# Kernel optimization log

Measured on AMD Instinct MI355X. Metric: run time of the kernel, lower is better.

The kernel has to match this reference:

```python
import math
import jax, jax.numpy as jnp
import numpy as np

B, H, W, C = 16, 64, 64, 192
WS, SHIFT, NH = 16, 8, 6
D = C // NH
N = WS * WS
HID = 4 * C
EPS = 1e-5


def _static_tables():
    # relative position index (N, N)
    coords = np.stack(np.meshgrid(np.arange(WS), np.arange(WS), indexing='ij'))  # (2, WS, WS)
    cf = coords.reshape(2, -1)
    rel = (cf[:, :, None] - cf[:, None, :]).transpose(1, 2, 0)  # (N, N, 2)
    rel[:, :, 0] += WS - 1
    rel[:, :, 1] += WS - 1
    rel[:, :, 0] *= 2 * WS - 1
    rel_idx = rel.sum(-1)  # (N, N)
    # log-spaced continuous relative coords table ((2WS-1)^2, 2)
    r = np.arange(-(WS - 1), WS, dtype=np.float32)
    tab = np.stack(np.meshgrid(r, r, indexing='ij'), axis=-1)  # (2WS-1, 2WS-1, 2)
    tab = tab / (WS - 1) * 8.0
    tab = np.sign(tab) * np.log2(np.abs(tab) + 1.0) / np.log2(8.0)
    # shifted-window attention mask (nW, N, N)
    img = np.zeros((H, W))
    cnt = 0
    for hs in (slice(0, -WS), slice(-WS, -SHIFT), slice(-SHIFT, None)):
        for ws_ in (slice(0, -WS), slice(-WS, -SHIFT), slice(-SHIFT, None)):
            img[hs, ws_] = cnt
            cnt += 1
    win = img.reshape(H // WS, WS, W // WS, WS).transpose(0, 2, 1, 3).reshape(-1, N)
    diff = win[:, None, :] - win[:, :, None]
    mask = np.where(diff != 0, -100.0, 0.0).astype(np.float32)
    return jnp.asarray(rel_idx), jnp.asarray(tab.reshape(-1, 2)), jnp.asarray(mask)

REL_IDX, CPB_TABLE, ATTN_MASK = _static_tables()


def setup_inputs() -> dict:
    key = jax.random.key(0)
    ks = jax.random.split(key, 24)
    s = 0.02
    return {
        'hidden_states': jax.random.normal(ks[0], (B, H * W, C), jnp.float32),
        'time': jax.random.uniform(ks[1], (B,), jnp.float32),
        'q_w': jax.random.normal(ks[2], (C, C), jnp.float32) * s,
        'q_b': jnp.zeros((C,), jnp.float32),
        'k_w': jax.random.normal(ks[3], (C, C), jnp.float32) * s,
        'v_w': jax.random.normal(ks[4], (C, C), jnp.float32) * s,
        'v_b': jnp.zeros((C,), jnp.float32),
        'logit_scale': jnp.full((NH, 1, 1), math.log(10.0), jnp.float32),
        'cpb_w1': jax.random.normal(ks[5], (512, 2), jnp.float32) * s,
        'cpb_b1': jnp.zeros((512,), jnp.float32),
        'cpb_w2': jax.random.normal(ks[6], (NH, 512), jnp.float32) * s,
        'proj_w': jax.random.normal(ks[7], (C, C), jnp.float32) * s,
        'proj_b': jnp.zeros((C,), jnp.float32),
        'ln1_ww': jax.random.normal(ks[8], (C, 1), jnp.float32) * s,
        'ln1_wb': jnp.ones((C,), jnp.float32),
        'ln1_bw': jax.random.normal(ks[9], (C, 1), jnp.float32) * s,
        'ln1_bb': jnp.zeros((C,), jnp.float32),
        'fc1_w': jax.random.normal(ks[10], (HID, C), jnp.float32) * s,
        'fc1_b': jnp.zeros((HID,), jnp.float32),
        'fc2_w': jax.random.normal(ks[11], (C, HID), jnp.float32) * s,
        'fc2_b': jnp.zeros((C,), jnp.float32),
        'ln2_ww': jax.random.normal(ks[12], (C, 1), jnp.float32) * s,
        'ln2_wb': jnp.ones((C,), jnp.float32),
        'ln2_bw': jax.random.normal(ks[13], (C, 1), jnp.float32) * s,
        'ln2_bb': jnp.zeros((C,), jnp.float32),
    }


def _cond_ln(x, time, ww, wb, bw, bb):
    mean = x.mean(-1, keepdims=True)
    var = (x ** 2).mean(-1, keepdims=True) - mean ** 2
    xn = (x - mean) / jnp.sqrt(var + EPS)
    t = time.reshape(-1, 1)
    w = (t @ ww.T + wb)[:, None, :]
    b = (t @ bw.T + bb)[:, None, :]
    return w * xn + b


def _forward(hidden_states, time, q_w, q_b, k_w, v_w, v_b, logit_scale,
             cpb_w1, cpb_b1, cpb_w2, proj_w, proj_b,
             ln1_ww, ln1_wb, ln1_bw, ln1_bb,
             fc1_w, fc1_b, fc2_w, fc2_b,
             ln2_ww, ln2_wb, ln2_bw, ln2_bb):
    nWh, nWw = H // WS, W // WS
    nW = nWh * nWw
    x = hidden_states.reshape(B, H, W, C)
    x = jnp.roll(x, (-SHIFT, -SHIFT), axis=(1, 2))
    # window partition -> (B*nW, N, C)
    xw = x.reshape(B, nWh, WS, nWw, WS, C).transpose(0, 1, 3, 2, 4, 5).reshape(-1, N, C)
    q = (xw @ q_w.T + q_b).reshape(-1, N, NH, D).transpose(0, 2, 1, 3)
    k = (xw @ k_w.T).reshape(-1, N, NH, D).transpose(0, 2, 1, 3)
    v = (xw @ v_w.T + v_b).reshape(-1, N, NH, D).transpose(0, 2, 1, 3)
    # cosine attention with learned temperature
    qn = q / jnp.linalg.norm(q, axis=-1, keepdims=True)
    kn = k / jnp.linalg.norm(k, axis=-1, keepdims=True)
    scale = jnp.exp(jnp.minimum(logit_scale, math.log(100.0)))  # (NH,1,1)
    attn = jnp.einsum('whnd,whmd->whnm', qn, kn) * scale
    # continuous relative position bias
    tbl = jnp.maximum(CPB_TABLE @ cpb_w1.T + cpb_b1, 0.0) @ cpb_w2.T  # (M, NH)
    rpb = tbl[REL_IDX.reshape(-1)].reshape(N, N, NH).transpose(2, 0, 1)
    attn = attn + 16.0 * jax.nn.sigmoid(rpb)[None]
    # shifted-window mask
    attn = attn.reshape(B, nW, NH, N, N) + ATTN_MASK[None, :, None]
    attn = jax.nn.softmax(attn.reshape(-1, NH, N, N), axis=-1)
    out = jnp.einsum('whnm,whmd->whnd', attn, v).transpose(0, 2, 1, 3).reshape(-1, N, C)
    out = out @ proj_w.T + proj_b
    # window reverse + un-roll
    out = out.reshape(B, nWh, nWw, WS, WS, C).transpose(0, 1, 3, 2, 4, 5).reshape(B, H, W, C)
    out = jnp.roll(out, (SHIFT, SHIFT), axis=(1, 2)).reshape(B, H * W, C)
    # res-post-norm residual blocks
    h = hidden_states + _cond_ln(out, time, ln1_ww, ln1_wb, ln1_bw, ln1_bb)
    mlp = jax.nn.gelu(h @ fc1_w.T + fc1_b, approximate=False) @ fc2_w.T + fc2_b
    return h + _cond_ln(mlp, time, ln2_ww, ln2_wb, ln2_bw, ln2_bb)


def reference(hidden_states, time, q_w, q_b, k_w, v_w, v_b, logit_scale,
              cpb_w1, cpb_b1, cpb_w2, proj_w, proj_b,
              ln1_ww, ln1_wb, ln1_bw, ln1_bb,
              fc1_w, fc1_b, fc2_w, fc2_b,
              ln2_ww, ln2_wb, ln2_bw, ln2_bb):
    return _forward(hidden_states, time, q_w, q_b, k_w, v_w, v_b, logit_scale,
                    cpb_w1, cpb_b1, cpb_w2, proj_w, proj_b,
                    ln1_ww, ln1_wb, ln1_bw, ln1_bb,
                    fc1_w, fc1_b, fc2_w, fc2_b,
                    ln2_ww, ln2_wb, ln2_bw, ln2_bb)
```

## Files before the change

kernel.cpp:

```cpp
#include <hip/hip_runtime.h>
#include <hip/hip_bf16.h>
#include <hip/hip_fp16.h>
#include <math.h>

#define BB 16
#define CC 192
#define SHIFT 8
#define NH 6
#define DD 32
#define NN 256
#define HID 768
#define NWIN 256
#define NROWS 65536

#define OFF_TBL   0ll
#define OFF_BIASM (32ll<<10)
#define OFF_WQKV  (3200ll<<10)
#define OFF_PWB   (3424ll<<10)
#define OFF_W1B   (3500ll<<10)
#define OFF_W2B   (3800ll<<10)
#define OFF_BQKV  (4096ll<<10)
#define OFF_WTAB  (4104ll<<10)
#define OFF_XB    (8ll<<20)
#define OFF_Q     (32ll<<20)
#define OFF_K     (56ll<<20)
#define OFF_V     (80ll<<20)
#define OFF_AO    (104ll<<20)
#define OFF_HB    OFF_XB

typedef __attribute__((ext_vector_type(4)))  float f32x4;
typedef __attribute__((ext_vector_type(16))) float f32x16;
typedef __attribute__((ext_vector_type(8)))  short bf16x8;

__device__ __forceinline__ void gload16(const void* g, void* l) {
    __builtin_amdgcn_global_load_lds(
        (const __attribute__((address_space(1))) void*)g,
        (__attribute__((address_space(3))) void*)l, 16, 0, 0);
}

__device__ __forceinline__ float b2f(short s) {
    unsigned u = ((unsigned)(unsigned short)s) << 16;
    return __builtin_bit_cast(float, u);
}
__device__ __forceinline__ short f2b(float f) {
    return __builtin_bit_cast(short, __float2bfloat16(f));
}
__device__ __forceinline__ unsigned pk2(float lo, float hi) {
    unsigned a = (unsigned short)f2b(lo);
    unsigned b = (unsigned short)f2b(hi);
    return a | (b << 16);
}

__device__ __forceinline__ float fexp2(float x) {
#if __has_builtin(__builtin_amdgcn_exp2f)
    return __builtin_amdgcn_exp2f(x);
#else
    return __expf(x * 0.69314718056f);
#endif
}

__device__ __forceinline__ float gelu_fast(float x) {
    float x2 = x * x;
    float z = x * fmaf(0.0713548353f, x2, 1.5957691216f);
    float e = __expf(-z);
    return x * __builtin_amdgcn_rcpf(1.0f + e);
}

__device__ __forceinline__ float cpb_coord(int u) {
    float t = (float)u * (8.0f / 15.0f);
    return copysignf(log2f(fabsf(t) + 1.0f) * (1.0f / 3.0f), t);
}

__global__ __launch_bounds__(512) void k_tbl(
    const float* __restrict__ w1, const float* __restrict__ b1,
    const float* __restrict__ w2, float* __restrict__ tbl)
{
    __shared__ float r[512];
    int m = blockIdx.x;
    int a = m / 31, b = m % 31;
    float c0 = cpb_coord(a - 15);
    float c1 = cpb_coord(b - 15);
    int hd = threadIdx.x;
    float rv = c0 * w1[hd * 2 + 0] + c1 * w1[hd * 2 + 1] + b1[hd];
    r[hd] = fmaxf(rv, 0.0f);
    __syncthreads();
    if (hd < NH) {
        float s = 0.0f;
        for (int k = 0; k < 512; ++k) s += r[k] * w2[hd * 512 + k];
        tbl[m * NH + hd] = s;
    }
}

__global__ __launch_bounds__(256) void k_biasm(
    const float* __restrict__ tbl, const float* __restrict__ lscale,
    __half* __restrict__ biasp)
{
    int bid = blockIdx.x;
    int ty = bid / (NH * NN);
    int rem = bid % (NH * NN);
    int h = rem >> 8, i = rem & 255;
    int j = threadIdx.x;
    int yi = i >> 4, xi = i & 15, yj = j >> 4, xj = j & 15;
    int idx = (yi - yj + 15) * 31 + (xi - xj + 15);
    float v = 16.0f / (1.0f + __expf(-tbl[idx * NH + h]));
    int rhi = (ty & 2) ? ((yi < SHIFT) ? 1 : 2) : 0;
    int rwi = (ty & 1) ? ((xi < SHIFT) ? 1 : 2) : 0;
    int rhj = (ty & 2) ? ((yj < SHIFT) ? 1 : 2) : 0;
    int rwj = (ty & 1) ? ((xj < SHIFT) ? 1 : 2) : 0;
    if (rhi * 3 + rwi != rhj * 3 + rwj) v -= 100.0f;
    float scale = __expf(fminf(lscale[h], 4.6051702f));
    v = (v - 16.0f - scale) * 1.44269504f;
    int jc = j & 31;
    int r = (jc & 3) + 4 * (jc >> 3);
    int g = (jc >> 2) & 1;
    int pos = (j & ~31) + g * 16 + r;
    biasp[(((size_t)ty * NH + h) * NN + i) * NN + pos] = __float2half(v);
}

__global__ __launch_bounds__(256) void k_cvt(
    const float* __restrict__ qw, const float* __restrict__ kw,
    const float* __restrict__ vw, const float* __restrict__ pw,
    const float* __restrict__ fc1w, const float* __restrict__ fc2w,
    const float* __restrict__ q_b, const float* __restrict__ v_b,
    __hip_bfloat16* __restrict__ wqkv, __hip_bfloat16* __restrict__ pwb,
    __hip_bfloat16* __restrict__ w1b, __hip_bfloat16* __restrict__ w2b,
    float* __restrict__ bqkv)
{
    int i = blockIdx.x * 256 + threadIdx.x;
    const int S1 = 36864, S2 = 73728, S3 = 110592, S4 = 147456,
              S5 = 294912, S6 = 442368, S7 = 442944;
    if (i < S3) {
        const float* src = (i < S1) ? qw : (i < S2) ? kw : vw;
        int off = (i < S1) ? i : (i < S2) ? i - S1 : i - S2;
        wqkv[i] = __float2bfloat16(src[off]);
    } else if (i < S4) { pwb[i - S3] = __float2bfloat16(pw[i - S3]); }
    else if (i < S5)   { w1b[i - S4] = __float2bfloat16(fc1w[i - S4]); }
    else if (i < S6)   { w2b[i - S5] = __float2bfloat16(fc2w[i - S5]); }
    else if (i < S7) {
        int j = i - S6;
        bqkv[j] = (j < 192) ? q_b[j] : (j < 384) ? 0.0f : v_b[j - 384];
    }
}

__global__ __launch_bounds__(256) void k_wtab(
    const float* __restrict__ time,
    const float* __restrict__ w1w, const float* __restrict__ w1b_,
    const float* __restrict__ b1w, const float* __restrict__ b1b_,
    const float* __restrict__ w2w, const float* __restrict__ w2b_,
    const float* __restrict__ b2w, const float* __restrict__ b2b_,
    float* __restrict__ wtab)
{
    int idx = blockIdx.x * 256 + threadIdx.x;
    int t = idx / 3072, rem = idx % 3072;
    int b = rem / 192, c = rem % 192;
    float tm = time[b];
    float v;
    if (t == 0)      v = tm * w1w[c] + w1b_[c];
    else if (t == 1) v = tm * b1w[c] + b1b_[c];
    else if (t == 2) v = tm * w2w[c] + w2b_[c];
    else             v = tm * b2w[c] + b2b_[c];
    wtab[idx] = v;
}

__global__ __launch_bounds__(256) void k_gather(
    const float* __restrict__ x, __hip_bfloat16* __restrict__ xb)
{
    int idx = blockIdx.x * 256 + threadIdx.x;
    int r = idx / 48, c4 = idx % 48;
    int win = r >> 8, n = r & 255;
    int b = win >> 4, wh = (win >> 2) & 3, ww = win & 3;
    int yi = n >> 4, xi = n & 15;
    int sy = (wh * 16 + yi + SHIFT) & 63;
    int sx = (ww * 16 + xi + SHIFT) & 63;
    float4 v = *(const float4*)&x[((size_t)b * 4096 + sy * 64 + sx) * CC + c4 * 4];
    union { short h[4]; short4 s4; } u;
    u.h[0] = f2b(v.x); u.h[1] = f2b(v.y); u.h[2] = f2b(v.z); u.h[3] = f2b(v.w);
    *(short4*)&((short*)xb)[(size_t)r * CC + c4 * 4] = u.s4;
}

#define STAGE_SWZ(dstLds, srcPtr, ldK, nR)                                  \
    for (int r_ = 0; r_ < (nR); ++r_) {                                     \
        int off_ = r_ * 256 + tid;                                          \
        int row_ = off_ >> 3, cb_ = off_ & 7;                               \
        int ce_ = ((cb_ ^ (row_ & 7)) << 3);                                \
        gload16((srcPtr) + (size_t)row_ * (ldK) + ce_, &(dstLds)[off_ * 8]); \
    }

__global__ __launch_bounds__(256) void k_qkvgemm(
    const __hip_bfloat16* __restrict__ A, const __hip_bfloat16* __restrict__ Bw,
    const float* __restrict__ bias, const float* __restrict__ lscale,
    __hip_bfloat16* __restrict__ qbo, __hip_bfloat16* __restrict__ kbo,
    __hip_bfloat16* __restrict__ vbo)
{
    __shared__ short lds[12288];
    short* As = lds;
    short* Bs = lds + 8192;
    int tid = threadIdx.x, lane = tid & 63;
    int w = tid >> 6, wr = w >> 1, wc = w & 1;
    int bm = blockIdx.x, bn = blockIdx.y;

    f32x4 acc[4][2];
    #pragma unroll
    for (int fm = 0; fm < 4; ++fm)
        #pragma unroll
        for (int fn = 0; fn < 2; ++fn) acc[fm][fn] = (f32x4)0.0f;

    for (int kt = 0; kt < CC; kt += 64) {
        STAGE_SWZ(As, A + (size_t)(bm * 128) * CC + kt, CC, 4)
        STAGE_SWZ(Bs, Bw + (size_t)(bn * 64) * CC + kt, CC, 2)
        __syncthreads();
        #pragma unroll
        for (int kk = 0; kk < 2; ++kk) {
            int kcq = kk * 4 + (lane >> 4);
            bf16x8 af[4], bfr[2];
            #pragma unroll
            for (int fm = 0; fm < 4; ++fm) {
                int row = wr * 64 + fm * 16 + (lane & 15);
                af[fm] = *(const bf16x8*)&As[row * 64 + ((kcq ^ (row & 7)) << 3)];
            }
            #pragma unroll
            for (int fn = 0; fn < 2; ++fn) {
                int row = wc * 32 + fn * 16 + (lane & 15);
                bfr[fn] = *(const bf16x8*)&Bs[row * 64 + ((kcq ^ (row & 7)) << 3)];
            }
            #pragma unroll
            for (int fm = 0; fm < 4; ++fm)
                #pragma unroll
                for (int fn = 0; fn < 2; ++fn)
                    acc[fm][fn] = __builtin_amdgcn_mfma_f32_16x16x32_bf16(
                        af[fm], bfr[fn], acc[fm][fn], 0, 0, 0);
        }
        __syncthreads();
    }

    bool donorm = (bn < 6);
    bool isq = (bn < 3);
    float qscale = __expf(fminf(lscale[(bn % 3) * 2 + wc], 4.6051702f)) * 1.44269504f;
    int bcol = bn * 64 + wc * 32 + (lane & 15);
    #pragma unroll
    for (int fm = 0; fm < 4; ++fm)
        #pragma unroll
        for (int r = 0; r < 4; ++r) {
            float v0 = acc[fm][0][r] + bias[bcol];
            float v1 = acc[fm][1][r] + bias[bcol + 16];
            if (donorm) {
                float s2 = v0 * v0 + v1 * v1;
                s2 += __shfl_xor(s2, 1);
                s2 += __shfl_xor(s2, 2);
                s2 += __shfl_xor(s2, 4);
                s2 += __shfl_xor(s2, 8);
                float rn = rsqrtf(s2);
                if (isq) rn *= qscale;
                v0 *= rn; v1 *= rn;
            }
            int rowl = wr * 64 + fm * 16 + ((lane >> 4) << 2) + r;
            int c0 = wc * 32 + (lane & 15);
            int sw = (rowl & 3) << 4;
            lds[rowl * 64 + (c0 ^ sw)] = f2b(v0);
            lds[rowl * 64 + ((c0 + 16) ^ sw)] = f2b(v1);
        }
    __syncthreads();
    __hip_bfloat16* dst = (bn < 3) ? qbo : (bn < 6) ? kbo : vbo;
    int cb0 = (bn % 3) * 64;
    #pragma unroll
    for (int rr = 0; rr < 2; ++rr) {
        int row = rr * 64 + (tid >> 2);
        int cl = (tid & 3) * 16;
        int cp = cl ^ ((row & 3) << 4);
        bf16x8 a = *(const bf16x8*)&lds[row * 64 + cp];
        bf16x8 b = *(const bf16x8*)&lds[row * 64 + cp + 8];
        size_t base = (size_t)(bm * 128 + row) * CC + cb0 + cl;
        *(bf16x8*)&dst[base] = a;
        *(bf16x8*)&dst[base + 8] = b;
    }
}

#define VTP 260
__global__ __launch_bounds__(256, 3) void k_attn(
    const __hip_bfloat16* __restrict__ qb,
    const __hip_bfloat16* __restrict__ kb,
    const __hip_bfloat16* __restrict__ vb,
    const __half* __restrict__ biasp,
    __hip_bfloat16* __restrict__ ao)
{
    __shared__ short Vt[32 * VTP];
    int blk = blockIdx.x;
    int win = blk / NH, h = blk % NH;
    int wwh = (win >> 2) & 3, www = win & 3;
    int ty = (((wwh == 3) ? 2 : 0) | ((www == 3) ? 1 : 0));
    int tid = threadIdx.x;
    int wv = tid >> 6, lane = tid & 63;
    int c = lane & 31, g = lane >> 5;

    {
        int j = wv * 64 + lane;
        const short* vsrc = (const short*)vb + ((size_t)(win * NN + j)) * CC + h * DD;
        #pragma unroll
        for (int q4 = 0; q4 < 4; ++q4) {
            bf16x8 t = *(const bf16x8*)(vsrc + q4 * 8);
            #pragma unroll
            for (int e = 0; e < 8; ++e)
                Vt[(q4 * 8 + e) * VTP + j] = t[e];
        }
    }
    __syncthreads();

    const short* qsrc = (const short*)qb + ((size_t)(win * NN + wv * 64)) * CC + h * DD;
    bf16x8 qf[2][2];
    #pragma unroll
    for (int fq = 0; fq < 2; ++fq)
        #pragma unroll
        for (int kd = 0; kd < 2; ++kd)
            qf[fq][kd] = *(const bf16x8*)(qsrc + (size_t)(32 * fq + c) * CC + 16 * kd + 8 * g);

    f32x16 acc_o[2];
    acc_o[0] = (f32x16)0.0f; acc_o[1] = (f32x16)0.0f;
    float lsum[2] = {0.0f, 0.0f};

    const short* kbase = (const short*)kb + ((size_t)(win * NN)) * CC + h * DD;
    const __half* bbase = biasp + (((size_t)ty * NH + h) * NN) * NN;

    for (int t = 0; t < 4; ++t) {
        int jt = t * 64;
        #pragma unroll
        for (int fj = 0; fj < 2; ++fj) {
            int jb = jt + 32 * fj;
            bf16x8 kf0 = *(const bf16x8*)(kbase + (size_t)(jb + c) * CC + 8 * g);
            bf16x8 kf1 = *(const bf16x8*)(kbase + (size_t)(jb + c) * CC + 16 + 8 * g);
            f32x16 st[2];
            __builtin_amdgcn_s_setprio(1);
            {
                f32x16 t0 = __builtin_amdgcn_mfma_f32_32x32x16_bf16(
                    kf0, qf[0][0], (f32x16)0.0f, 0, 0, 0);
                st[0] = __builtin_amdgcn_mfma_f32_32x32x16_bf16(
                    kf1, qf[0][1], t0, 0, 0, 0);
                f32x16 t1 = __builtin_amdgcn_mfma_f32_32x32x16_bf16(
                    kf0, qf[1][0], (f32x16)0.0f, 0, 0, 0);
                st[1] = __builtin_amdgcn_mfma_f32_32x32x16_bf16(
                    kf1, qf[1][1], t1, 0, 0, 0);
            }
            __builtin_amdgcn_s_setprio(0);
            bf16x8 vfr[2];
            #pragma unroll
            for (int rb = 0; rb < 2; ++rb) {
                int j0 = jb + 16 * rb + 4 * g;
                uint2 va = *(const uint2*)&Vt[c * VTP + j0];
                uint2 vb2 = *(const uint2*)&Vt[c * VTP + j0 + 8];
                union { unsigned u[4]; bf16x8 v; } vu;
                vu.u[0] = va.x; vu.u[1] = va.y; vu.u[2] = vb2.x; vu.u[3] = vb2.y;
                vfr[rb] = vu.v;
            }
            #pragma unroll
            for (int fq = 0; fq < 2; ++fq) {
                const __half* bp = bbase + (size_t)(wv * 64 + 32 * fq + c) * NN
                                   + jb + g * 16;
                union { uint4 u; __half2 h2[4]; } ba, bbu;
                ba.u  = *(const uint4*)bp;
                bbu.u = *(const uint4*)(bp + 8);
                float p[16];
                #pragma unroll
                for (int q4 = 0; q4 < 4; ++q4) {
                    float2 fa = __half22float2(ba.h2[q4]);
                    p[2 * q4 + 0] = st[fq][2 * q4 + 0] + fa.x;
                    p[2 * q4 + 1] = st[fq][2 * q4 + 1] + fa.y;
                    float2 fb = __half22float2(bbu.h2[q4]);
                    p[8 + 2 * q4 + 0] = st[fq][8 + 2 * q4 + 0] + fb.x;
                    p[8 + 2 * q4 + 1] = st[fq][8 + 2 * q4 + 1] + fb.y;
                }
                #pragma unroll
                for (int r = 0; r < 16; ++r) p[r] = fexp2(p[r]);
                #pragma unroll
                for (int r = 0; r < 16; ++r) lsum[fq] += p[r];
                union { unsigned u[4]; bf16x8 v; } pu0, pu1;
                pu0.u[0] = pk2(p[0],  p[1]);  pu0.u[1] = pk2(p[2],  p[3]);
                pu0.u[2] = pk2(p[4],  p[5]);  pu0.u[3] = pk2(p[6],  p[7]);
                pu1.u[0] = pk2(p[8],  p[9]);  pu1.u[1] = pk2(p[10], p[11]);
                pu1.u[2] = pk2(p[12], p[13]); pu1.u[3] = pk2(p[14], p[15]);
                __builtin_amdgcn_s_setprio(1);
                acc_o[fq] = __builtin_amdgcn_mfma_f32_32x32x16_bf16(
                    pu0.v, vfr[0], acc_o[fq], 0, 0, 0);
                acc_o[fq] = __builtin_amdgcn_mfma_f32_32x32x16_bf16(
                    pu1.v, vfr[1], acc_o[fq], 0, 0, 0);
                __builtin_amdgcn_s_setprio(0);
            }
        }
    }

    #pragma unroll
    for (int fq = 0; fq < 2; ++fq) {
        lsum[fq] += __shfl_xor(lsum[fq], 32);
        float rlv = 1.0f / lsum[fq];
        #pragma unroll
        for (int r = 0; r < 16; ++r) {
            int rho = (r & 3) + 8 * (r >> 2) + 4 * g;
            float rli = __shfl(rlv, rho);
            int row = wv * 64 + 32 * fq + rho;
            ao[((size_t)(win * NN + row)) * CC + h * DD + c] =
                __float2bfloat16(acc_o[fq][r] * rli);
        }
    }
}

__global__ __launch_bounds__(256) void k_projgemm(
    const __hip_bfloat16* __restrict__ ao,
    const __hip_bfloat16* __restrict__ pwb,
    const float* __restrict__ pbias,
    const float* __restrict__ wtab,
    __hip_bfloat16* xbhb)
{
    __shared__ short lds[25600];
    __shared__ float part[128][4];
    short* As = lds;
    short* Bs = lds + 8192;
    int tid = threadIdx.x, lane = tid & 63;
    int w = tid >> 6, wr = w >> 1, wc = w & 1;
    int bm = blockIdx.x;

    f32x4 acc[4][6];
    #pragma unroll
    for (int fm = 0; fm < 4; ++fm)
        #pragma unroll
        for (int fn = 0; fn < 6; ++fn) acc[fm][fn] = (f32x4)0.0f;

    for (int kt = 0; kt < CC; kt += 64) {
        STAGE_SWZ(As, ao + (size_t)(bm * 128) * CC + kt, CC, 4)
        STAGE_SWZ(Bs, pwb + kt, CC, 6)
        __syncthreads();
        #pragma unroll
        for (int kk = 0; kk < 2; ++kk) {
            int kcq = kk * 4 + (lane >> 4);
            bf16x8 af[4], bfr[6];
            #pragma unroll
            for (int fm = 0; fm < 4; ++fm) {
                int row = wr * 64 + fm * 16 + (lane & 15);
                af[fm] = *(const bf16x8*)&As[row * 64 + ((kcq ^ (row & 7)) << 3)];
            }
            #pragma unroll
            for (int fn = 0; fn < 6; ++fn) {
                int row = wc * 96 + fn * 16 + (lane & 15);
                bfr[fn] = *(const bf16x8*)&Bs[row * 64 + ((kcq ^ (row & 7)) << 3)];
            }
            #pragma unroll
            for (int fm = 0; fm < 4; ++fm)
                #pragma unroll
                for (int fn = 0; fn < 6; ++fn)
                    acc[fm][fn] = __builtin_amdgcn_mfma_f32_16x16x32_bf16(
                        af[fm], bfr[fn], acc[fm][fn], 0, 0, 0);
        }
        __syncthreads();
    }

    #pragma unroll
    for (int fm = 0; fm < 4; ++fm)
        #pragma unroll
        for (int r = 0; r < 4; ++r) {
            int rowl = wr * 64 + fm * 16 + ((lane >> 4) << 2) + r;
            float s = 0.0f, s2 = 0.0f;
            #pragma unroll
            for (int fn = 0; fn < 6; ++fn) {
                int col = wc * 96 + fn * 16 + (lane & 15);
                float v = acc[fm][fn][r] + pbias[col];
                lds[rowl * 200 + col] = f2b(v);
                s += v; s2 += v * v;
            }
            #pragma unroll
            for (int m = 1; m < 16; m <<= 1) {
                s  += __shfl_xor(s, m);
                s2 += __shfl_xor(s2, m);
            }
            if ((lane & 15) == 0) {
                part[rowl][wc * 2]     = s;
                part[rowl][wc * 2 + 1] = s2;
            }
        }
    __syncthreads();

    int row = tid >> 1;
    int cb = (tid & 1) * 96;
    float s  = part[row][0] + part[row][2];
    float s2 = part[row][1] + part[row][3];
    float mean = s * (1.0f / 192.0f);
    float rstd = rsqrtf(s2 * (1.0f / 192.0f) - mean * mean + 1e-5f);
    int rw = bm * 128 + row;
    const float* wt = wtab + (rw >> 12) * 192;
    const float* bt = wtab + 16 * 192 + (rw >> 12) * 192;
    #pragma unroll
    for (int c8 = 0; c8 < 12; ++c8) {
        int c = cb + c8 * 8;
        bf16x8 lv = *(const bf16x8*)&lds[row * 200 + c];
        bf16x8 xv = *(const bf16x8*)&xbhb[(size_t)rw * CC + c];
        float4 w0 = *(const float4*)&wt[c], w1 = *(const float4*)&wt[c + 4];
        float4 b0 = *(const float4*)&bt[c], b1 = *(const float4*)&bt[c + 4];
        float wv[8] = {w0.x, w0.y, w0.z, w0.w, w1.x, w1.y, w1.z, w1.w};
        float bv[8] = {b0.x, b0.y, b0.z, b0.w, b1.x, b1.y, b1.z, b1.w};
        bf16x8 o;
        #pragma unroll
        for (int e = 0; e < 8; ++e) {
            float xn = (b2f(lv[e]) - mean) * rstd;
            o[e] = f2b(b2f(xv[e]) + wv[e] * xn + bv[e]);
        }
        *(bf16x8*)&xbhb[(size_t)rw * CC + c] = o;
    }
}

__global__ __launch_bounds__(256, 2) void k_mlp(
    const __hip_bfloat16* __restrict__ hb,
    const __hip_bfloat16* __restrict__ w1b,
    const float* __restrict__ b1,
    const __hip_bfloat16* __restrict__ w2b,
    const float* __restrict__ b2,
    const float* __restrict__ wtab,
    float* __restrict__ out)
{
    __shared__ short lds[40960];
    short* As  = lds;
    short* W1c = lds + 12288;
    short* H2c = lds + 24576;
    short* W2c = lds + 28672;
    short* VAL = lds + 12288;
    float* part = (float*)&lds[28672];

    int tid = threadIdx.x, lane = tid & 63;
    int w = tid >> 6, wr = w >> 1, wc = w & 1;
    int bm = blockIdx.x;
    size_t rb = (size_t)bm * 64;

    #pragma unroll
    for (int kt = 0; kt < 3; ++kt)
        STAGE_SWZ(As + kt * 4096, hb + rb * CC + kt * 64, CC, 2)

    f32x4 acc2[2][6];
    #pragma unroll
    for (int fm = 0; fm < 2; ++fm)
        #pragma unroll
        for (int fn = 0; fn < 6; ++fn) acc2[fm][fn] = (f32x4)0.0f;

    for (int it = 0; it < 12; ++it) {
        __syncthreads();
        #pragma unroll
        for (int kt = 0; kt < 3; ++kt)
            STAGE_SWZ(W1c + kt * 4096, w1b + (size_t)(it * 64) * CC + kt * 64, CC, 2)
        STAGE_SWZ(W2c, w2b + it * 64, HID, 6)
        __syncthreads();

        f32x4 acc1[2][2];
        #pragma unroll
        for (int fm = 0; fm < 2; ++fm)
            #pragma unroll
            for (int fn = 0; fn < 2; ++fn) acc1[fm][fn] = (f32x4)0.0f;
        #pragma unroll
        for (int kt = 0; kt < 3; ++kt)
            #pragma unroll
            for (int kk = 0; kk < 2; ++kk) {
                int kcq = kk * 4 + (lane >> 4);
                bf16x8 af[2], bfr[2];
                #pragma unroll
                for (int fm = 0; fm < 2; ++fm) {
                    int row = wr * 32 + fm * 16 + (lane & 15);
                    af[fm] = *(const bf16x8*)&As[kt * 4096 + row * 64 + ((kcq ^ (row & 7)) << 3)];
                }
                #pragma unroll
                for (int fn = 0; fn < 2; ++fn) {
                    int row = wc * 32 + fn * 16 + (lane & 15);
                    bfr[fn] = *(const bf16x8*)&W1c[kt * 4096 + row * 64 + ((kcq ^ (row & 7)) << 3)];
                }
                #pragma unroll
                for (int fm = 0; fm < 2; ++fm)
                    #pragma unroll
                    for (int fn = 0; fn < 2; ++fn)
                        acc1[fm][fn] = __builtin_amdgcn_mfma_f32_16x16x32_bf16(
                            af[fm], bfr[fn], acc1[fm][fn], 0, 0, 0);
            }
        #pragma unroll
        for (int fm = 0; fm < 2; ++fm)
            #pragma unroll
            for (int fn = 0; fn < 2; ++fn) {
                int coll = wc * 32 + fn * 16 + (lane & 15);
                float bv = b1[it * 64 + coll];
                #pragma unroll
                for (int r = 0; r < 4; ++r) {
                    int rowl = wr * 32 + fm * 16 + ((lane >> 4) << 2) + r;
                    float v = gelu_fast(acc1[fm][fn][r] + bv);
                    H2c[rowl * 64 + (((coll >> 3) ^ (rowl & 7)) << 3) + (coll & 7)] = f2b(v);
                }
            }
        __syncthreads();

        #pragma unroll
        for (int kk = 0; kk < 2; ++kk) {
            int kcq = kk * 4 + (lane >> 4);
            bf16x8 af[2], bfr[6];
            #pragma unroll
            for (int fm = 0; fm < 2; ++fm) {
                int row = wr * 32 + fm * 16 + (lane & 15);
                af[fm] = *(const bf16x8*)&H2c[row * 64 + ((kcq ^ (row & 7)) << 3)];
            }
            #pragma unroll
            for (int fn = 0; fn < 6; ++fn) {
                int row = wc * 96 + fn * 16 + (lane & 15);
                bfr[fn] = *(const bf16x8*)&W2c[row * 64 + ((kcq ^ (row & 7)) << 3)];
            }
            #pragma unroll
            for (int fm = 0; fm < 2; ++fm)
                #pragma unroll
                for (int fn = 0; fn < 6; ++fn)
                    acc2[fm][fn] = __builtin_amdgcn_mfma_f32_16x16x32_bf16(
                        af[fm], bfr[fn], acc2[fm][fn], 0, 0, 0);
        }
    }
    __syncthreads();

    #pragma unroll
    for (int fm = 0; fm < 2; ++fm)
        #pragma unroll
        for (int r = 0; r < 4; ++r) {
            int rowl = wr * 32 + fm * 16 + ((lane >> 4) << 2) + r;
            float s = 0.0f, s2 = 0.0f;
            #pragma unroll
            for (int fn = 0; fn < 6; ++fn) {
                int col = wc * 96 + fn * 16 + (lane & 15);
                float v = acc2[fm][fn][r] + b2[col];
                VAL[rowl * 200 + col] = f2b(v);
                s += v; s2 += v * v;
            }
            #pragma unroll
            for (int m = 1; m < 16; m <<= 1) {
                s  += __shfl_xor(s, m);
                s2 += __shfl_xor(s2, m);
            }
            if ((lane & 15) == 0) {
                part[rowl * 4 + wc * 2]     = s;
                part[rowl * 4 + wc * 2 + 1] = s2;
            }
        }
    __syncthreads();

    int row = tid >> 2;
    int cb = (tid & 3) * 48;
    float s  = part[row * 4 + 0] + part[row * 4 + 2];
    float s2 = part[row * 4 + 1] + part[row * 4 + 3];
    float mean = s * (1.0f / 192.0f);
    float rstd = rsqrtf(s2 * (1.0f / 192.0f) - mean * mean + 1e-5f);
    int rw = (int)rb + row;
    int win = rw >> 8, n = rw & 255, b = rw >> 12;
    int wh = (win >> 2) & 3, wwn = win & 3;
    int y  = (wh * 16 + (n >> 4) + SHIFT) & 63;
    int xq = (wwn * 16 + (n & 15) + SHIFT) & 63;
    size_t rimg = (size_t)b * 4096 + y * 64 + xq;
    const float* wt = wtab + 2 * 16 * 192 + b * 192;
    const float* bt = wtab + 3 * 16 * 192 + b * 192;
    #pragma unroll
    for (int c8 = 0; c8 < 6; ++c8) {
        int c = cb + c8 * 8;
        bf16x8 lv = *(const bf16x8*)&VAL[row * 200 + c];
        bf16x8 hv = *(const bf16x8*)&As[(c >> 6) * 4096 + row * 64 +
                                        ((((c & 63) >> 3) ^ (row & 7)) << 3)];
        float4 w0 = *(const float4*)&wt[c], w1 = *(const float4*)&wt[c + 4];
        float4 b0 = *(const float4*)&bt[c], b1 = *(const float4*)&bt[c + 4];
        float wv[8] = {w0.x, w0.y, w0.z, w0.w, w1.x, w1.y, w1.z, w1.w};
        float bv[8] = {b0.x, b0.y, b0.z, b0.w, b1.x, b1.y, b1.z, b1.w};
        float4 o0, o1;
        float oo[8];
        #pragma unroll
        for (int e = 0; e < 8; ++e) {
            float xn = (b2f(lv[e]) - mean) * rstd;
            oo[e] = b2f(hv[e]) + wv[e] * xn + bv[e];
        }
        o0.x = oo[0]; o0.y = oo[1]; o0.z = oo[2]; o0.w = oo[3];
        o1.x = oo[4]; o1.y = oo[5]; o1.z = oo[6]; o1.w = oo[7];
        *(float4*)&out[rimg * CC + c] = o0;
        *(float4*)&out[rimg * CC + c + 4] = o1;
    }
}

extern "C" void kernel_launch(void* const* d_in, const int* in_sizes, int n_in,
                              void* d_out, int out_size, void* d_ws, size_t ws_size,
                              hipStream_t stream)
{
    const float* x        = (const float*)d_in[0];
    const float* time     = (const float*)d_in[1];
    const float* q_w      = (const float*)d_in[2];
    const float* q_b      = (const float*)d_in[3];
    const float* k_w      = (const float*)d_in[4];
    const float* v_w      = (const float*)d_in[5];
    const float* v_b      = (const float*)d_in[6];
    const float* lscale   = (const float*)d_in[7];
    const float* cpb_w1   = (const float*)d_in[8];
    const float* cpb_b1   = (const float*)d_in[9];
    const float* cpb_w2   = (const float*)d_in[10];
    const float* proj_w   = (const float*)d_in[11];
    const float* proj_b   = (const float*)d_in[12];
    const float* ln1_ww   = (const float*)d_in[13];
    const float* ln1_wb   = (const float*)d_in[14];
    const float* ln1_bw   = (const float*)d_in[15];
    const float* ln1_bb   = (const float*)d_in[16];
    const float* fc1_w    = (const float*)d_in[17];
    const float* fc1_b    = (const float*)d_in[18];
    const float* fc2_w    = (const float*)d_in[19];
    const float* fc2_b    = (const float*)d_in[20];
    const float* ln2_ww   = (const float*)d_in[21];
    const float* ln2_wb   = (const float*)d_in[22];
    const float* ln2_bw   = (const float*)d_in[23];
    const float* ln2_bb   = (const float*)d_in[24];

    char* ws = (char*)d_ws;
    float* tbl            = (float*)(ws + OFF_TBL);
    __half* biasp         = (__half*)(ws + OFF_BIASM);
    __hip_bfloat16* wqkv  = (__hip_bfloat16*)(ws + OFF_WQKV);
    __hip_bfloat16* pwb   = (__hip_bfloat16*)(ws + OFF_PWB);
    __hip_bfloat16* w1b   = (__hip_bfloat16*)(ws + OFF_W1B);
    __hip_bfloat16* w2b   = (__hip_bfloat16*)(ws + OFF_W2B);
    float* bqkv           = (float*)(ws + OFF_BQKV);
    float* wtab           = (float*)(ws + OFF_WTAB);
    __hip_bfloat16* xb    = (__hip_bfloat16*)(ws + OFF_XB);
    __hip_bfloat16* qb    = (__hip_bfloat16*)(ws + OFF_Q);
    __hip_bfloat16* kb    = (__hip_bfloat16*)(ws + OFF_K);
    __hip_bfloat16* vb    = (__hip_bfloat16*)(ws + OFF_V);
    __hip_bfloat16* ao    = (__hip_bfloat16*)(ws + OFF_AO);
    __hip_bfloat16* hb    = (__hip_bfloat16*)(ws + OFF_HB);
    float* out            = (float*)d_out;

    k_tbl   <<<961, 512, 0, stream>>>(cpb_w1, cpb_b1, cpb_w2, tbl);
    k_biasm <<<4 * NH * NN, 256, 0, stream>>>(tbl, lscale, biasp);
    k_cvt   <<<1731, 256, 0, stream>>>(q_w, k_w, v_w, proj_w, fc1_w, fc2_w,
                                       q_b, v_b, wqkv, pwb, w1b, w2b, bqkv);
    k_wtab  <<<48, 256, 0, stream>>>(time, ln1_ww, ln1_wb, ln1_bw, ln1_bb,
                                     ln2_ww, ln2_wb, ln2_bw, ln2_bb, wtab);
    k_gather<<<12288, 256, 0, stream>>>(x, xb);
    k_qkvgemm<<<dim3(NROWS / 128, 9), 256, 0, stream>>>(xb, wqkv, bqkv, lscale, qb, kb, vb);
    k_attn  <<<NWIN * NH, 256, 0, stream>>>(qb, kb, vb, biasp, ao);
    k_projgemm<<<NROWS / 128, 256, 0, stream>>>(ao, pwb, proj_b, wtab, xb);
    k_mlp   <<<NROWS / 64, 256, 0, stream>>>(hb, w1b, fc1_b, w2b, fc2_b, wtab, out);
}
```

Before: 230.4 us.

## Double MLP block tile to 128 rows with 512 threads and split epilogue

The fused MLP kernel now processes 128 rows per block with 8 waves instead of 64 rows with 4 waves. Each fc1/fc2 weight chunk staged into LDS is therefore reused across twice as many rows, halving weight staging traffic per row. To fit LDS, the layer-norm epilogue keeps fc2 results in registers and writes them to LDS in two column halves, adding extra barriers. The larger LDS footprint limits co-resident blocks per CU.

```diff
diff --git a/kernel.cpp b/kernel.cpp
--- a/kernel.cpp
+++ b/kernel.cpp
@@ -186,6 +186,14 @@
         gload16((srcPtr) + (size_t)row_ * (ldK) + ce_, &(dstLds)[off_ * 8]); \
     }
 
+#define STAGE_SWZ5(dstLds, srcPtr, ldK, nR)                                 \
+    for (int r_ = 0; r_ < (nR); ++r_) {                                     \
+        int off_ = r_ * 512 + tid;                                          \
+        int row_ = off_ >> 3, cb_ = off_ & 7;                               \
+        int ce_ = ((cb_ ^ (row_ & 7)) << 3);                                \
+        gload16((srcPtr) + (size_t)row_ * (ldK) + ce_, &(dstLds)[off_ * 8]); \
+    }
+
 __global__ __launch_bounds__(256) void k_qkvgemm(
     const __hip_bfloat16* __restrict__ A, const __hip_bfloat16* __restrict__ Bw,
     const float* __restrict__ bias, const float* __restrict__ lscale,
@@ -503,7 +511,7 @@
     }
 }
 
-__global__ __launch_bounds__(256, 2) void k_mlp(
+__global__ __launch_bounds__(512, 2) void k_mlp(
     const __hip_bfloat16* __restrict__ hb,
     const __hip_bfloat16* __restrict__ w1b,
     const float* __restrict__ b1,
@@ -512,22 +520,22 @@
     const float* __restrict__ wtab,
     float* __restrict__ out)
 {
-    __shared__ short lds[40960];
+    __shared__ short lds[57344];
     short* As  = lds;
-    short* W1c = lds + 12288;
-    short* H2c = lds + 24576;
-    short* W2c = lds + 28672;
-    short* VAL = lds + 12288;
-    float* part = (float*)&lds[28672];
+    short* W1c = lds + 24576;
+    short* H2c = lds + 36864;
+    short* W2c = lds + 45056;
+    short* VAL = lds + 24576;
+    float* part = (float*)&lds[45056];
 
     int tid = threadIdx.x, lane = tid & 63;
     int w = tid >> 6, wr = w >> 1, wc = w & 1;
     int bm = blockIdx.x;
-    size_t rb = (size_t)bm * 64;
+    size_t rb = (size_t)bm * 128;
 
     #pragma unroll
     for (int kt = 0; kt < 3; ++kt)
-        STAGE_SWZ(As + kt * 4096, hb + rb * CC + kt * 64, CC, 2)
+        STAGE_SWZ5(As + kt * 8192, hb + rb * CC + kt * 64, CC, 2)
 
     f32x4 acc2[2][6];
     #pragma unroll
@@ -539,8 +547,8 @@
         __syncthreads();
         #pragma unroll
         for (int kt = 0; kt < 3; ++kt)
-            STAGE_SWZ(W1c + kt * 4096, w1b + (size_t)(it * 64) * CC + kt * 64, CC, 2)
-        STAGE_SWZ(W2c, w2b + it * 64, HID, 6)
+            STAGE_SWZ5(W1c + kt * 4096, w1b + (size_t)(it * 64) * CC + kt * 64, CC, 1)
+        STAGE_SWZ5(W2c, w2b + it * 64, HID, 3)
         __syncthreads();
 
         f32x4 acc1[2][2];
@@ -557,7 +565,7 @@
                 #pragma unroll
                 for (int fm = 0; fm < 2; ++fm) {
                     int row = wr * 32 + fm * 16 + (lane & 15);
-                    af[fm] = *(const bf16x8*)&As[kt * 4096 + row * 64 + ((kcq ^ (row & 7)) << 3)];
+                    af[fm] = *(const bf16x8*)&As[kt * 8192 + row * 64 + ((kcq ^ (row & 7)) << 3)];
                 }
                 #pragma unroll
                 for (int fn = 0; fn < 2; ++fn) {
@@ -620,7 +628,7 @@
             for (int fn = 0; fn < 6; ++fn) {
                 int col = wc * 96 + fn * 16 + (lane & 15);
                 float v = acc2[fm][fn][r] + b2[col];
-                VAL[rowl * 200 + col] = f2b(v);
+                acc2[fm][fn][r] = v;
                 s += v; s2 += v * v;
             }
             #pragma unroll
@@ -636,7 +644,7 @@
     __syncthreads();
 
     int row = tid >> 2;
-    int cb = (tid & 3) * 48;
+    int cseg = (tid & 3) * 24;
     float s  = part[row * 4 + 0] + part[row * 4 + 2];
     float s2 = part[row * 4 + 1] + part[row * 4 + 3];
     float mean = s * (1.0f / 192.0f);
@@ -649,27 +657,47 @@
     size_t rimg = (size_t)b * 4096 + y * 64 + xq;
     const float* wt = wtab + 2 * 16 * 192 + b * 192;
     const float* bt = wtab + 3 * 16 * 192 + b * 192;
-    #pragma unroll
-    for (int c8 = 0; c8 < 6; ++c8) {
-        int c = cb + c8 * 8;
-        bf16x8 lv = *(const bf16x8*)&VAL[row * 200 + c];
-        bf16x8 hv = *(const bf16x8*)&As[(c >> 6) * 4096 + row * 64 +
-                                        ((((c & 63) >> 3) ^ (row & 7)) << 3)];
-        float4 w0 = *(const float4*)&wt[c], w1 = *(const float4*)&wt[c + 4];
-        float4 b0 = *(const float4*)&bt[c], b1 = *(const float4*)&bt[c + 4];
-        float wv[8] = {w0.x, w0.y, w0.z, w0.w, w1.x, w1.y, w1.z, w1.w};
-        float bv[8] = {b0.x, b0.y, b0.z, b0.w, b1.x, b1.y, b1.z, b1.w};
-        float4 o0, o1;
-        float oo[8];
-        #pragma unroll
-        for (int e = 0; e < 8; ++e) {
-            float xn = (b2f(lv[e]) - mean) * rstd;
-            oo[e] = b2f(hv[e]) + wv[e] * xn + bv[e];
-        }
-        o0.x = oo[0]; o0.y = oo[1]; o0.z = oo[2]; o0.w = oo[3];
-        o1.x = oo[4]; o1.y = oo[5]; o1.z = oo[6]; o1.w = oo[7];
-        *(float4*)&out[rimg * CC + c] = o0;
-        *(float4*)&out[rimg * CC + c + 4] = o1;
+
+    #pragma unroll
+    for (int cc = 0; cc < 2; ++cc) {
+        if (wc == cc) {
+            #pragma unroll
+            for (int fm = 0; fm < 2; ++fm)
+                #pragma unroll
+                for (int fn = 0; fn < 6; ++fn) {
+                    int colv = fn * 16 + (lane & 15);
+                    #pragma unroll
+                    for (int r = 0; r < 4; ++r) {
+                        int rowl = wr * 32 + fm * 16 + ((lane >> 4) << 2) + r;
+                        VAL[rowl * 104 + colv] = f2b(acc2[fm][fn][r]);
+                    }
+                }
+        }
+        __syncthreads();
+        #pragma unroll
+        for (int c8 = 0; c8 < 3; ++c8) {
+            int c = cseg + c8 * 8;
+            int gc = cc * 96 + c;
+            bf16x8 lv = *(const bf16x8*)&VAL[row * 104 + c];
+            bf16x8 hv = *(const bf16x8*)&As[(gc >> 6) * 8192 + row * 64 +
+                                            ((((gc & 63) >> 3) ^ (row & 7)) << 3)];
+            float4 w0 = *(const float4*)&wt[gc], w1 = *(const float4*)&wt[gc + 4];
+            float4 b0 = *(const float4*)&bt[gc], b1 = *(const float4*)&bt[gc + 4];
+            float wv[8] = {w0.x, w0.y, w0.z, w0.w, w1.x, w1.y, w1.z, w1.w};
+            float bv[8] = {b0.x, b0.y, b0.z, b0.w, b1.x, b1.y, b1.z, b1.w};
+            float4 o0, o1;
+            float oo[8];
+            #pragma unroll
+            for (int e = 0; e < 8; ++e) {
+                float xn = (b2f(lv[e]) - mean) * rstd;
+                oo[e] = b2f(hv[e]) + wv[e] * xn + bv[e];
+            }
+            o0.x = oo[0]; o0.y = oo[1]; o0.z = oo[2]; o0.w = oo[3];
+            o1.x = oo[4]; o1.y = oo[5]; o1.z = oo[6]; o1.w = oo[7];
+            *(float4*)&out[rimg * CC + gc] = o0;
+            *(float4*)&out[rimg * CC + gc + 4] = o1;
+        }
+        __syncthreads();
     }
 }
 
@@ -730,5 +758,5 @@
     k_qkvgemm<<<dim3(NROWS / 128, 9), 256, 0, stream>>>(xb, wqkv, bqkv, lscale, qb, kb, vb);
     k_attn  <<<NWIN * NH, 256, 0, stream>>>(qb, kb, vb, biasp, ao);
     k_projgemm<<<NROWS / 128, 256, 0, stream>>>(ao, pwb, proj_b, wtab, xb);
-    k_mlp   <<<NROWS / 64, 256, 0, stream>>>(hb, w1b, fc1_b, w2b, fc2_b, wtab, out);
-}
+    k_mlp   <<<NROWS / 128, 512, 0, stream>>>(hb, w1b, fc1_b, w2b, fc2_b, wtab, out);
+}
```

New measurement: 238.2 us. +3.4%, slower.

## Load MLP operands directly from global into registers, double-buffer hidden tile

Applied to the files above, without the earlier changes.

The fused MLP kernel no longer stages the input rows or the W1/W2 weight tiles through LDS. A-operand fragments are held in registers for the whole kernel, and weight fragments are read straight from global memory (served by cache) each iteration. The GELU hidden tile is double-buffered in LDS, which removes the barriers around weight staging. LDS usage falls enough to raise the occupancy target to 3 blocks per SM. In exchange it adds register pressure from the persistent fragments and uncoalesced, repeated global loads of the weights.

```diff
diff --git a/kernel.cpp b/kernel.cpp
--- a/kernel.cpp
+++ b/kernel.cpp
@@ -503,7 +503,7 @@
     }
 }
 
-__global__ __launch_bounds__(256, 2) void k_mlp(
+__global__ __launch_bounds__(256, 3) void k_mlp(
     const __hip_bfloat16* __restrict__ hb,
     const __hip_bfloat16* __restrict__ w1b,
     const float* __restrict__ b1,
@@ -512,22 +512,31 @@
     const float* __restrict__ wtab,
     float* __restrict__ out)
 {
-    __shared__ short lds[40960];
-    short* As  = lds;
-    short* W1c = lds + 12288;
-    short* H2c = lds + 24576;
-    short* W2c = lds + 28672;
-    short* VAL = lds + 12288;
-    float* part = (float*)&lds[28672];
+    __shared__ short lds[12800];
+    __shared__ float part[64][4];
+    short* H2c = lds;
+    short* VAL = lds;
 
     int tid = threadIdx.x, lane = tid & 63;
     int w = tid >> 6, wr = w >> 1, wc = w & 1;
     int bm = blockIdx.x;
     size_t rb = (size_t)bm * 64;
 
+    const short* hsrc = (const short*)hb;
+    const short* w1s = (const short*)w1b;
+    const short* w2s = (const short*)w2b;
+
+    bf16x8 afr[3][2][2];
     #pragma unroll
     for (int kt = 0; kt < 3; ++kt)
-        STAGE_SWZ(As + kt * 4096, hb + rb * CC + kt * 64, CC, 2)
+        #pragma unroll
+        for (int kk = 0; kk < 2; ++kk)
+            #pragma unroll
+            for (int fm = 0; fm < 2; ++fm) {
+                int row = wr * 32 + fm * 16 + (lane & 15);
+                int kof = kt * 64 + kk * 32 + (lane >> 4) * 8;
+                afr[kt][kk][fm] = *(const bf16x8*)(hsrc + (rb + row) * CC + kof);
+            }
 
     f32x4 acc2[2][6];
     #pragma unroll
@@ -535,41 +544,30 @@
         #pragma unroll
         for (int fn = 0; fn < 6; ++fn) acc2[fm][fn] = (f32x4)0.0f;
 
+    int buf = 0;
     for (int it = 0; it < 12; ++it) {
-        __syncthreads();
+        f32x4 acc1[2][2];
+        #pragma unroll
+        for (int fm = 0; fm < 2; ++fm)
+            #pragma unroll
+            for (int fn = 0; fn < 2; ++fn) acc1[fm][fn] = (f32x4)0.0f;
         #pragma unroll
         for (int kt = 0; kt < 3; ++kt)
-            STAGE_SWZ(W1c + kt * 4096, w1b + (size_t)(it * 64) * CC + kt * 64, CC, 2)
-        STAGE_SWZ(W2c, w2b + it * 64, HID, 6)
-        __syncthreads();
-
-        f32x4 acc1[2][2];
-        #pragma unroll
-        for (int fm = 0; fm < 2; ++fm)
-            #pragma unroll
-            for (int fn = 0; fn < 2; ++fn) acc1[fm][fn] = (f32x4)0.0f;
-        #pragma unroll
-        for (int kt = 0; kt < 3; ++kt)
             #pragma unroll
             for (int kk = 0; kk < 2; ++kk) {
-                int kcq = kk * 4 + (lane >> 4);
-                bf16x8 af[2], bfr[2];
-                #pragma unroll
-                for (int fm = 0; fm < 2; ++fm) {
-                    int row = wr * 32 + fm * 16 + (lane & 15);
-                    af[fm] = *(const bf16x8*)&As[kt * 4096 + row * 64 + ((kcq ^ (row & 7)) << 3)];
-                }
+                bf16x8 bfr[2];
                 #pragma unroll
                 for (int fn = 0; fn < 2; ++fn) {
-                    int row = wc * 32 + fn * 16 + (lane & 15);
-                    bfr[fn] = *(const bf16x8*)&W1c[kt * 4096 + row * 64 + ((kcq ^ (row & 7)) << 3)];
+                    int row = it * 64 + wc * 32 + fn * 16 + (lane & 15);
+                    int kof = kt * 64 + kk * 32 + (lane >> 4) * 8;
+                    bfr[fn] = *(const bf16x8*)(w1s + (size_t)row * CC + kof);
                 }
                 #pragma unroll
                 for (int fm = 0; fm < 2; ++fm)
                     #pragma unroll
                     for (int fn = 0; fn < 2; ++fn)
                         acc1[fm][fn] = __builtin_amdgcn_mfma_f32_16x16x32_bf16(
-                            af[fm], bfr[fn], acc1[fm][fn], 0, 0, 0);
+                            afr[kt][kk][fm], bfr[fn], acc1[fm][fn], 0, 0, 0);
             }
         #pragma unroll
         for (int fm = 0; fm < 2; ++fm)
@@ -581,7 +579,8 @@
                 for (int r = 0; r < 4; ++r) {
                     int rowl = wr * 32 + fm * 16 + ((lane >> 4) << 2) + r;
                     float v = gelu_fast(acc1[fm][fn][r] + bv);
-                    H2c[rowl * 64 + (((coll >> 3) ^ (rowl & 7)) << 3) + (coll & 7)] = f2b(v);
+                    H2c[buf * 4096 + rowl * 64 +
+                        (((coll >> 3) ^ (rowl & 7)) << 3) + (coll & 7)] = f2b(v);
                 }
             }
         __syncthreads();
@@ -593,12 +592,13 @@
             #pragma unroll
             for (int fm = 0; fm < 2; ++fm) {
                 int row = wr * 32 + fm * 16 + (lane & 15);
-                af[fm] = *(const bf16x8*)&H2c[row * 64 + ((kcq ^ (row & 7)) << 3)];
+                af[fm] = *(const bf16x8*)&H2c[buf * 4096 + row * 64 + ((kcq ^ (row & 7)) << 3)];
             }
             #pragma unroll
             for (int fn = 0; fn < 6; ++fn) {
                 int row = wc * 96 + fn * 16 + (lane & 15);
-                bfr[fn] = *(const bf16x8*)&W2c[row * 64 + ((kcq ^ (row & 7)) << 3)];
+                int kof = it * 64 + kk * 32 + (lane >> 4) * 8;
+                bfr[fn] = *(const bf16x8*)(w2s + (size_t)row * HID + kof);
             }
             #pragma unroll
             for (int fm = 0; fm < 2; ++fm)
@@ -607,6 +607,7 @@
                     acc2[fm][fn] = __builtin_amdgcn_mfma_f32_16x16x32_bf16(
                         af[fm], bfr[fn], acc2[fm][fn], 0, 0, 0);
         }
+        buf ^= 1;
     }
     __syncthreads();
 
@@ -629,16 +630,16 @@
                 s2 += __shfl_xor(s2, m);
             }
             if ((lane & 15) == 0) {
-                part[rowl * 4 + wc * 2]     = s;
-                part[rowl * 4 + wc * 2 + 1] = s2;
+                part[rowl][wc * 2]     = s;
+                part[rowl][wc * 2 + 1] = s2;
             }
         }
     __syncthreads();
 
     int row = tid >> 2;
     int cb = (tid & 3) * 48;
-    float s  = part[row * 4 + 0] + part[row * 4 + 2];
-    float s2 = part[row * 4 + 1] + part[row * 4 + 3];
+    float s  = part[row][0] + part[row][2];
+    float s2 = part[row][1] + part[row][3];
     float mean = s * (1.0f / 192.0f);
     float rstd = rsqrtf(s2 * (1.0f / 192.0f) - mean * mean + 1e-5f);
     int rw = (int)rb + row;
@@ -653,8 +654,7 @@
     for (int c8 = 0; c8 < 6; ++c8) {
         int c = cb + c8 * 8;
         bf16x8 lv = *(const bf16x8*)&VAL[row * 200 + c];
-        bf16x8 hv = *(const bf16x8*)&As[(c >> 6) * 4096 + row * 64 +
-                                        ((((c & 63) >> 3) ^ (row & 7)) << 3)];
+        bf16x8 hv = *(const bf16x8*)(hsrc + (size_t)rw * CC + c);
         float4 w0 = *(const float4*)&wt[c], w1 = *(const float4*)&wt[c + 4];
         float4 b0 = *(const float4*)&bt[c], b1 = *(const float4*)&bt[c + 4];
         float wv[8] = {w0.x, w0.y, w0.z, w0.w, w1.x, w1.y, w1.z, w1.w};
```

New measurement: 361.2 us. 56.8% more time.
